# Kernel tuning notes

Hardware: AMD Instinct MI355X
Metric: run time of the kernel (lower is better)

The kernel has to match this reference:

```python
import jax, jax.numpy as jnp
import numpy as np

DIM = 768
HEAD_DIM = 768


def setup_inputs() -> dict:
    key = jax.random.key(0)
    k_x, k_w, k_b = jax.random.split(key, 3)
    x = jax.random.normal(k_x, (4, 4096, DIM), dtype=jnp.float32)
    # torch Linear(dim, 3*head_dim): weight [3H, dim]; store transposed [dim, 3H]
    scale = 1.0 / np.sqrt(DIM)
    W_qkv = jax.random.uniform(k_w, (DIM, 3 * HEAD_DIM), dtype=jnp.float32,
                               minval=-scale, maxval=scale)
    b_qkv = jax.random.uniform(k_b, (3 * HEAD_DIM,), dtype=jnp.float32,
                               minval=-scale, maxval=scale)
    return {"x": x, "W_qkv": W_qkv, "b_qkv": b_qkv}


def reference(x, W_qkv, b_qkv):
    # x: [B, N, C]
    qkv = jnp.einsum("bnc,ch->bnh", x, W_qkv) + b_qkv  # [B, N, 3H]
    q, k, v = jnp.split(qkv, 3, axis=-1)               # each [B, N, H]
    H = q.shape[-1]
    scores = jnp.einsum("bnh,bmh->bnm", q, k) / jnp.sqrt(jnp.float32(H))
    attn = jax.nn.softmax(scores, axis=-1)             # [B, N, N]
    out = jnp.einsum("bnm,bmh->bnh", attn, v)          # [B, N, H]
    return out
```

## Files before the change

kernel.cpp:

```cpp
#include <hip/hip_runtime.h>
#include <stdint.h>

typedef __attribute__((ext_vector_type(8))) short short8;
typedef __attribute__((ext_vector_type(4))) float f32x4;

#define DIM 768
#define H3 2304
#define SEQ 4096
#define NTOK 16384

__device__ __forceinline__ unsigned short f2bf(float f) {
  union { float f; uint32_t u; } c; c.f = f;
  uint32_t u = c.u;
  u += 0x7FFFu + ((u >> 16) & 1u);
  return (unsigned short)(u >> 16);
}

__device__ __forceinline__ void async_cp16(const void* g, void* l) {
  __builtin_amdgcn_global_load_lds(
      (__attribute__((address_space(1))) void*)(void*)g,
      (__attribute__((address_space(3))) void*)l, 16, 0, 0);
}

__device__ __forceinline__ void gemm_nt64(
    const unsigned short* __restrict__ A, const unsigned short* __restrict__ B,
    int K, int ldA, int ldB,
    unsigned short* As, unsigned short* Bs, f32x4 acc[4][4])
{
  const int tid = threadIdx.x, lane = tid & 63, wid = tid >> 6;
  const int wm = (wid & 1) << 6, wn = (wid >> 1) << 6;
  const int lr = lane & 15, q = lane >> 4;

#pragma unroll
  for (int i = 0; i < 4; ++i)
#pragma unroll
    for (int j = 0; j < 4; ++j)
      acc[i][j] = (f32x4){0.f, 0.f, 0.f, 0.f};

  const unsigned short* gA[4];
  const unsigned short* gB[4];
#pragma unroll
  for (int t = 0; t < 4; ++t) {
    const int c = tid + 256 * t;
    const int row = c >> 3, sc = c & 7;
    const int col8 = ((sc ^ (row & 7)) << 3);
    gA[t] = A + (size_t)row * ldA + col8;
    gB[t] = B + (size_t)row * ldB + col8;
  }

  for (int k0 = 0; k0 < K; k0 += 64) {
#pragma unroll
    for (int t = 0; t < 4; ++t)
      async_cp16(gA[t] + k0, As + (tid + 256 * t) * 8);
#pragma unroll
    for (int t = 0; t < 4; ++t)
      async_cp16(gB[t] + k0, Bs + (tid + 256 * t) * 8);
    __syncthreads();

    short8 af[4][2], bfr[4][2];
#pragma unroll
    for (int i = 0; i < 4; ++i) {
      const int ra = wm + i * 16 + lr;
#pragma unroll
      for (int s2 = 0; s2 < 2; ++s2)
        af[i][s2] = *(const short8*)(As + ra * 64 + (((s2 * 4 + q) ^ (ra & 7)) << 3));
    }
#pragma unroll
    for (int j = 0; j < 4; ++j) {
      const int rb = wn + j * 16 + lr;
#pragma unroll
      for (int s2 = 0; s2 < 2; ++s2)
        bfr[j][s2] = *(const short8*)(Bs + rb * 64 + (((s2 * 4 + q) ^ (rb & 7)) << 3));
    }
#pragma unroll
    for (int s2 = 0; s2 < 2; ++s2)
#pragma unroll
      for (int i = 0; i < 4; ++i)
#pragma unroll
        for (int j = 0; j < 4; ++j)
          acc[i][j] = __builtin_amdgcn_mfma_f32_16x16x32_bf16(af[i][s2], bfr[j][s2], acc[i][j], 0, 0, 0);
    __syncthreads();
  }
}

__global__ __launch_bounds__(256) void k_cvt(const float* __restrict__ in,
                                             unsigned short* __restrict__ o) {
  int i = blockIdx.x * 256 + threadIdx.x;
  float4 f = ((const float4*)in)[i];
  ushort4 u;
  u.x = f2bf(f.x); u.y = f2bf(f.y); u.z = f2bf(f.z); u.w = f2bf(f.w);
  ((ushort4*)o)[i] = u;
}

__global__ __launch_bounds__(256) void k_transpose(const float* __restrict__ W,
                                                   unsigned short* __restrict__ Wt) {
  __shared__ float tile[32][33];
  const int bc = blockIdx.x * 32;
  const int br = blockIdx.y * 32;
  const int tx = threadIdx.x & 31, ty = threadIdx.x >> 5;
#pragma unroll
  for (int i = 0; i < 32; i += 8)
    tile[ty + i][tx] = W[(size_t)(br + ty + i) * H3 + bc + tx];
  __syncthreads();
#pragma unroll
  for (int i = 0; i < 32; i += 8)
    Wt[(size_t)(bc + ty + i) * DIM + br + tx] = f2bf(tile[tx][ty + i]);
}

__global__ __launch_bounds__(256) void k_qkv(
    const unsigned short* __restrict__ xbf, const unsigned short* __restrict__ Wt,
    const float* __restrict__ bias,
    unsigned short* __restrict__ qb, unsigned short* __restrict__ kb,
    unsigned short* __restrict__ vT)
{
  __shared__ unsigned short As[128 * 64];
  __shared__ unsigned short Bs[128 * 64];
  f32x4 acc[4][4];
  const int g = blockIdx.x;
  const int xcd = g & 7, slot = g >> 3;
  const int tn = slot % 18, grp = slot / 18;
  const int tm = xcd + 8 * grp;
  gemm_nt64(xbf + (size_t)(tm * 128) * DIM, Wt + (size_t)(tn * 128) * DIM,
            DIM, DIM, DIM, As, Bs, acc);

  const int tid = threadIdx.x, lane = tid & 63, wid = tid >> 6;
  const int wm = (wid & 1) << 6, wn = (wid >> 1) << 6;
  const float scale = 0.036084391824351615f;
#pragma unroll
  for (int i = 0; i < 4; ++i) {
#pragma unroll
    for (int j = 0; j < 4; ++j) {
      const int col  = tn * 128 + wn + j * 16 + (lane & 15);
      const int row0 = tm * 128 + wm + i * 16 + ((lane >> 4) << 2);
      const float bc = bias[col];
#pragma unroll
      for (int r = 0; r < 4; ++r) {
        const int row = row0 + r;
        const float v = acc[i][j][r] + bc;
        if (col < 768) {
          qb[(size_t)row * DIM + col] = f2bf(v * scale);
        } else if (col < 1536) {
          kb[(size_t)row * DIM + (col - 768)] = f2bf(v);
        } else {
          const int b = row >> 12, n = row & 4095;
          vT[((size_t)b * DIM + (col - 1536)) * SEQ + n] = f2bf(v);
        }
      }
    }
  }
}

__global__ __launch_bounds__(256) void k_scores(
    const unsigned short* __restrict__ qb, const unsigned short* __restrict__ kb,
    unsigned short* __restrict__ S)
{
  __shared__ unsigned short As[128 * 64];
  __shared__ unsigned short Bs[128 * 64];
  f32x4 acc[4][4];
  const int g = blockIdx.x;
  const int xcd = g & 7, slot = g >> 3;
  const int tn = slot & 31, grp = slot >> 5;
  const int s  = xcd + 8 * grp;
  const int ty = s & 31, b = s >> 5;
  const unsigned short* A  = qb + (size_t)b * SEQ * DIM + (size_t)(ty * 128) * DIM;
  const unsigned short* Bm = kb + (size_t)b * SEQ * DIM + (size_t)(tn * 128) * DIM;
  unsigned short* Sb = S + (size_t)b * SEQ * SEQ;
  gemm_nt64(A, Bm, DIM, DIM, DIM, As, Bs, acc);

  const int tid = threadIdx.x, lane = tid & 63, wid = tid >> 6;
  const int wm = (wid & 1) << 6, wn = (wid >> 1) << 6;
#pragma unroll
  for (int i = 0; i < 4; ++i)
#pragma unroll
    for (int j = 0; j < 4; ++j) {
      const int col  = tn * 128 + wn + j * 16 + (lane & 15);
      const int row0 = ty * 128 + wm + i * 16 + ((lane >> 4) << 2);
#pragma unroll
      for (int r = 0; r < 4; ++r)
        Sb[(size_t)(row0 + r) * SEQ + col] = f2bf(acc[i][j][r]);
    }
}

__global__ __launch_bounds__(256) void k_softmax(unsigned short* __restrict__ S)
{
  const size_t base = (size_t)blockIdx.x * SEQ;
  uint4* rp = (uint4*)(S + base);
  const int t = threadIdx.x, lane = t & 63, wid = t >> 6;
  const uint4 cA = rp[t], cB = rp[t + 256];
  uint32_t wsv[8] = {cA.x, cA.y, cA.z, cA.w, cB.x, cB.y, cB.z, cB.w};
  float v[16];
#pragma unroll
  for (int i = 0; i < 8; ++i) {
    union { uint32_t u; float f; } lo, hi;
    lo.u = wsv[i] << 16; hi.u = wsv[i] & 0xFFFF0000u;
    v[2 * i] = lo.f; v[2 * i + 1] = hi.f;
  }
  float m = -1e30f;
#pragma unroll
  for (int i = 0; i < 16; ++i) m = fmaxf(m, v[i]);
#pragma unroll
  for (int off = 32; off > 0; off >>= 1) m = fmaxf(m, __shfl_down(m, off));
  __shared__ float redm[4], reds[4];
  if (lane == 0) redm[wid] = m;
  __syncthreads();
  m = fmaxf(fmaxf(redm[0], redm[1]), fmaxf(redm[2], redm[3]));
  float s = 0.f;
#pragma unroll
  for (int i = 0; i < 16; ++i) { v[i] = __expf(v[i] - m); s += v[i]; }
#pragma unroll
  for (int off = 32; off > 0; off >>= 1) s += __shfl_down(s, off);
  if (lane == 0) reds[wid] = s;
  __syncthreads();
  s = reds[0] + reds[1] + reds[2] + reds[3];
  const float inv = 1.0f / s;
  uint32_t o[8];
#pragma unroll
  for (int i = 0; i < 8; ++i)
    o[i] = (uint32_t)f2bf(v[2 * i] * inv) | ((uint32_t)f2bf(v[2 * i + 1] * inv) << 16);
  uint4 oA = {o[0], o[1], o[2], o[3]}, oB = {o[4], o[5], o[6], o[7]};
  rp[t] = oA; rp[t + 256] = oB;
}

__global__ __launch_bounds__(256) void k_pv(
    const unsigned short* __restrict__ P, const unsigned short* __restrict__ vT,
    float* __restrict__ out)
{
  __shared__ unsigned short As[128 * 64];
  __shared__ unsigned short Bs[128 * 64];
  f32x4 acc[4][4];
  const int g = blockIdx.x;
  const int xcd = g & 7, slot = g >> 3;
  const int tn = slot % 6, grp = slot / 6;
  const int s  = xcd + 8 * grp;
  const int ty = s & 31, b = s >> 5;

  const unsigned short* A  = P  + (size_t)b * SEQ * SEQ + (size_t)(ty * 128) * SEQ;
  const unsigned short* Bm = vT + (size_t)b * DIM * SEQ + (size_t)(tn * 128) * SEQ;
  float* ob = out + (size_t)b * SEQ * DIM;
  gemm_nt64(A, Bm, SEQ, SEQ, SEQ, As, Bs, acc);

  const int tid = threadIdx.x, lane = tid & 63, wid = tid >> 6;
  const int wm = (wid & 1) << 6, wn = (wid >> 1) << 6;
#pragma unroll
  for (int i = 0; i < 4; ++i)
#pragma unroll
    for (int j = 0; j < 4; ++j) {
      const int col  = tn * 128 + wn + j * 16 + (lane & 15);
      const int row0 = ty * 128 + wm + i * 16 + ((lane >> 4) << 2);
#pragma unroll
      for (int r = 0; r < 4; ++r)
        ob[(size_t)(row0 + r) * DIM + col] = acc[i][j][r];
    }
}

extern "C" void kernel_launch(void* const* d_in, const int* in_sizes, int n_in,
                              void* d_out, int out_size, void* d_ws, size_t ws_size,
                              hipStream_t stream) {
  const float* x    = (const float*)d_in[0];
  const float* W    = (const float*)d_in[1];
  const float* bias = (const float*)d_in[2];
  float* out = (float*)d_out;

  char* w = (char*)d_ws;
  unsigned short* x_bf = (unsigned short*)(w);
  unsigned short* Wt   = (unsigned short*)(w + 25165824);
  unsigned short* qb   = (unsigned short*)(w + 28704768);
  unsigned short* kb   = (unsigned short*)(w + 53870592);
  unsigned short* vT   = (unsigned short*)(w + 79036416);
  unsigned short* S    = (unsigned short*)(w + 104202240);

  k_cvt      <<<12288, 256, 0, stream>>>(x, x_bf);
  k_transpose<<<dim3(72, 24), 256, 0, stream>>>(W, Wt);
  k_qkv      <<<2304, 256, 0, stream>>>(x_bf, Wt, bias, qb, kb, vT);
  k_scores   <<<4096, 256, 0, stream>>>(qb, kb, S);
  k_softmax  <<<16384, 256, 0, stream>>>(S);
  k_pv       <<<768, 256, 0, stream>>>(S, vT, out);
}
```

Before: 512.0 us.

## Stage score tile through LDS for coalesced stores; split-K the PV GEMM

The scores kernel now writes its bf16 tile into padded shared memory and then stores it with 16-byte coalesced writes, replacing scattered 2-byte global stores. The PV GEMM is split into two halves along the key dimension, doubling the grid from 768 to 1536 blocks to fill more CUs. The second half writes to a scratch buffer that reuses the x_bf region, and an extra reduction kernel adds it into the output. This costs an extra pass over the fp32 output and one more launch.

```diff
diff --git a/kernel.cpp b/kernel.cpp
--- a/kernel.cpp
+++ b/kernel.cpp
@@ -150,12 +150,14 @@
   }
 }
 
+#define EP_LD 132
 __global__ __launch_bounds__(256) void k_scores(
     const unsigned short* __restrict__ qb, const unsigned short* __restrict__ kb,
     unsigned short* __restrict__ S)
 {
-  __shared__ unsigned short As[128 * 64];
-  __shared__ unsigned short Bs[128 * 64];
+  __shared__ unsigned short sm[128 * EP_LD];
+  unsigned short* As = sm;
+  unsigned short* Bs = sm + 128 * 64;
   f32x4 acc[4][4];
   const int g = blockIdx.x;
   const int xcd = g & 7, slot = g >> 3;
@@ -173,12 +175,20 @@
   for (int i = 0; i < 4; ++i)
 #pragma unroll
     for (int j = 0; j < 4; ++j) {
-      const int col  = tn * 128 + wn + j * 16 + (lane & 15);
-      const int row0 = ty * 128 + wm + i * 16 + ((lane >> 4) << 2);
+      const int col  = wn + j * 16 + (lane & 15);
+      const int row0 = wm + i * 16 + ((lane >> 4) << 2);
 #pragma unroll
       for (int r = 0; r < 4; ++r)
-        Sb[(size_t)(row0 + r) * SEQ + col] = f2bf(acc[i][j][r]);
-    }
+        sm[(row0 + r) * EP_LD + col] = f2bf(acc[i][j][r]);
+    }
+  __syncthreads();
+  const int rL = tid >> 4, cc = (tid & 15) << 3;
+#pragma unroll
+  for (int p = 0; p < 8; ++p) {
+    const int row = p * 16 + rL;
+    *(uint4*)(Sb + (size_t)(ty * 128 + row) * SEQ + tn * 128 + cc) =
+        *(const uint4*)(sm + row * EP_LD + cc);
+  }
 }
 
 __global__ __launch_bounds__(256) void k_softmax(unsigned short* __restrict__ S)
@@ -223,22 +233,23 @@
 
 __global__ __launch_bounds__(256) void k_pv(
     const unsigned short* __restrict__ P, const unsigned short* __restrict__ vT,
-    float* __restrict__ out)
+    float* __restrict__ out, float* __restrict__ part)
 {
   __shared__ unsigned short As[128 * 64];
   __shared__ unsigned short Bs[128 * 64];
   f32x4 acc[4][4];
   const int g = blockIdx.x;
   const int xcd = g & 7, slot = g >> 3;
-  const int tn = slot % 6, grp = slot / 6;
+  const int tn = slot % 6, t2 = slot / 6;
+  const int h = t2 & 1, grp = t2 >> 1;
   const int s  = xcd + 8 * grp;
   const int ty = s & 31, b = s >> 5;
 
-  const unsigned short* A  = P  + (size_t)b * SEQ * SEQ + (size_t)(ty * 128) * SEQ;
-  const unsigned short* Bm = vT + (size_t)b * DIM * SEQ + (size_t)(tn * 128) * SEQ;
-  float* ob = out + (size_t)b * SEQ * DIM;
-  gemm_nt64(A, Bm, SEQ, SEQ, SEQ, As, Bs, acc);
-
+  const unsigned short* A  = P  + (size_t)b * SEQ * SEQ + (size_t)(ty * 128) * SEQ + h * 2048;
+  const unsigned short* Bm = vT + (size_t)b * DIM * SEQ + (size_t)(tn * 128) * SEQ + h * 2048;
+  gemm_nt64(A, Bm, 2048, SEQ, SEQ, As, Bs, acc);
+
+  float* dst = (h ? part : out) + (size_t)b * SEQ * DIM;
   const int tid = threadIdx.x, lane = tid & 63, wid = tid >> 6;
   const int wm = (wid & 1) << 6, wn = (wid >> 1) << 6;
 #pragma unroll
@@ -249,8 +260,17 @@
       const int row0 = ty * 128 + wm + i * 16 + ((lane >> 4) << 2);
 #pragma unroll
       for (int r = 0; r < 4; ++r)
-        ob[(size_t)(row0 + r) * DIM + col] = acc[i][j][r];
-    }
+        dst[(size_t)(row0 + r) * DIM + col] = acc[i][j][r];
+    }
+}
+
+__global__ __launch_bounds__(256) void k_reduce(float* __restrict__ out,
+                                                const float* __restrict__ part) {
+  int i = blockIdx.x * 256 + threadIdx.x;
+  float4 a = ((const float4*)out)[i];
+  float4 p = ((const float4*)part)[i];
+  a.x += p.x; a.y += p.y; a.z += p.z; a.w += p.w;
+  ((float4*)out)[i] = a;
 }
 
 extern "C" void kernel_launch(void* const* d_in, const int* in_sizes, int n_in,
@@ -268,11 +288,13 @@
   unsigned short* kb   = (unsigned short*)(w + 53870592);
   unsigned short* vT   = (unsigned short*)(w + 79036416);
   unsigned short* S    = (unsigned short*)(w + 104202240);
+  float* part = (float*)(w);
 
   k_cvt      <<<12288, 256, 0, stream>>>(x, x_bf);
   k_transpose<<<dim3(72, 24), 256, 0, stream>>>(W, Wt);
   k_qkv      <<<2304, 256, 0, stream>>>(x_bf, Wt, bias, qb, kb, vT);
   k_scores   <<<4096, 256, 0, stream>>>(qb, kb, S);
   k_softmax  <<<16384, 256, 0, stream>>>(S);
-  k_pv       <<<768, 256, 0, stream>>>(S, vT, out);
-}
+  k_pv       <<<1536, 256, 0, stream>>>(S, vT, out, part);
+  k_reduce   <<<12288, 256, 0, stream>>>(out, part);
+}
```

Result: no change. 520.7 us (+1.7%).

## Fuse softmax exponentiation into score GEMM epilogue and defer normalization to PV

Applied to the files above, without the earlier changes.

Drops the separate softmax kernel. The score GEMM epilogue now applies exp to each score, accumulates per-row partial sums with atomics into a zeroed buffer, and writes the bf16 exponentials through an LDS-staged, coalesced store. The PV kernel divides its output rows by those sums. This removes a full read and write of the N×N score matrix. The cost is that exp is taken without subtracting the row max, which relies on the scores staying small enough not to overflow.

```diff
diff --git a/kernel.cpp b/kernel.cpp
--- a/kernel.cpp
+++ b/kernel.cpp
@@ -105,6 +105,10 @@
 #pragma unroll
   for (int i = 0; i < 32; i += 8)
     Wt[(size_t)(bc + ty + i) * DIM + br + tx] = f2bf(tile[tx][ty + i]);
+}
+
+__global__ __launch_bounds__(256) void k_zero(float* __restrict__ p) {
+  p[blockIdx.x * 256 + threadIdx.x] = 0.f;
 }
 
 __global__ __launch_bounds__(256) void k_qkv(
@@ -150,12 +154,14 @@
   }
 }
 
+#define EP_LD 132
 __global__ __launch_bounds__(256) void k_scores(
     const unsigned short* __restrict__ qb, const unsigned short* __restrict__ kb,
-    unsigned short* __restrict__ S)
-{
-  __shared__ unsigned short As[128 * 64];
-  __shared__ unsigned short Bs[128 * 64];
+    unsigned short* __restrict__ S, float* __restrict__ lsum)
+{
+  __shared__ unsigned short sm[128 * EP_LD];
+  unsigned short* As = sm;
+  unsigned short* Bs = sm + 128 * 64;
   f32x4 acc[4][4];
   const int g = blockIdx.x;
   const int xcd = g & 7, slot = g >> 3;
@@ -169,61 +175,47 @@
 
   const int tid = threadIdx.x, lane = tid & 63, wid = tid >> 6;
   const int wm = (wid & 1) << 6, wn = (wid >> 1) << 6;
-#pragma unroll
-  for (int i = 0; i < 4; ++i)
-#pragma unroll
-    for (int j = 0; j < 4; ++j) {
-      const int col  = tn * 128 + wn + j * 16 + (lane & 15);
-      const int row0 = ty * 128 + wm + i * 16 + ((lane >> 4) << 2);
-#pragma unroll
-      for (int r = 0; r < 4; ++r)
-        Sb[(size_t)(row0 + r) * SEQ + col] = f2bf(acc[i][j][r]);
-    }
-}
-
-__global__ __launch_bounds__(256) void k_softmax(unsigned short* __restrict__ S)
-{
-  const size_t base = (size_t)blockIdx.x * SEQ;
-  uint4* rp = (uint4*)(S + base);
-  const int t = threadIdx.x, lane = t & 63, wid = t >> 6;
-  const uint4 cA = rp[t], cB = rp[t + 256];
-  uint32_t wsv[8] = {cA.x, cA.y, cA.z, cA.w, cB.x, cB.y, cB.z, cB.w};
-  float v[16];
-#pragma unroll
-  for (int i = 0; i < 8; ++i) {
-    union { uint32_t u; float f; } lo, hi;
-    lo.u = wsv[i] << 16; hi.u = wsv[i] & 0xFFFF0000u;
-    v[2 * i] = lo.f; v[2 * i + 1] = hi.f;
-  }
-  float m = -1e30f;
-#pragma unroll
-  for (int i = 0; i < 16; ++i) m = fmaxf(m, v[i]);
-#pragma unroll
-  for (int off = 32; off > 0; off >>= 1) m = fmaxf(m, __shfl_down(m, off));
-  __shared__ float redm[4], reds[4];
-  if (lane == 0) redm[wid] = m;
+  const int q = lane >> 4;
+  float rs[4][4];
+#pragma unroll
+  for (int i = 0; i < 4; ++i) {
+#pragma unroll
+    for (int r = 0; r < 4; ++r) rs[i][r] = 0.f;
+#pragma unroll
+    for (int j = 0; j < 4; ++j) {
+      const int col  = wn + j * 16 + (lane & 15);
+      const int row0 = wm + i * 16 + (q << 2);
+#pragma unroll
+      for (int r = 0; r < 4; ++r) {
+        const float e = __expf(acc[i][j][r]);
+        sm[(row0 + r) * EP_LD + col] = f2bf(e);
+        rs[i][r] += e;
+      }
+    }
+  }
+  const int lbase = b * SEQ + ty * 128 + wm + (q << 2);
+#pragma unroll
+  for (int i = 0; i < 4; ++i)
+#pragma unroll
+    for (int r = 0; r < 4; ++r) {
+      float v = rs[i][r];
+      v += __shfl_xor(v, 1); v += __shfl_xor(v, 2);
+      v += __shfl_xor(v, 4); v += __shfl_xor(v, 8);
+      if ((lane & 15) == 0) atomicAdd(&lsum[lbase + i * 16 + r], v);
+    }
   __syncthreads();
-  m = fmaxf(fmaxf(redm[0], redm[1]), fmaxf(redm[2], redm[3]));
-  float s = 0.f;
-#pragma unroll
-  for (int i = 0; i < 16; ++i) { v[i] = __expf(v[i] - m); s += v[i]; }
-#pragma unroll
-  for (int off = 32; off > 0; off >>= 1) s += __shfl_down(s, off);
-  if (lane == 0) reds[wid] = s;
-  __syncthreads();
-  s = reds[0] + reds[1] + reds[2] + reds[3];
-  const float inv = 1.0f / s;
-  uint32_t o[8];
-#pragma unroll
-  for (int i = 0; i < 8; ++i)
-    o[i] = (uint32_t)f2bf(v[2 * i] * inv) | ((uint32_t)f2bf(v[2 * i + 1] * inv) << 16);
-  uint4 oA = {o[0], o[1], o[2], o[3]}, oB = {o[4], o[5], o[6], o[7]};
-  rp[t] = oA; rp[t + 256] = oB;
+  const int rL = tid >> 4, cc = (tid & 15) << 3;
+#pragma unroll
+  for (int p = 0; p < 8; ++p) {
+    const int row = p * 16 + rL;
+    *(uint4*)(Sb + (size_t)(ty * 128 + row) * SEQ + tn * 128 + cc) =
+        *(const uint4*)(sm + row * EP_LD + cc);
+  }
 }
 
 __global__ __launch_bounds__(256) void k_pv(
     const unsigned short* __restrict__ P, const unsigned short* __restrict__ vT,
-    float* __restrict__ out)
+    const float* __restrict__ lsum, float* __restrict__ out)
 {
   __shared__ unsigned short As[128 * 64];
   __shared__ unsigned short Bs[128 * 64];
@@ -241,15 +233,23 @@
 
   const int tid = threadIdx.x, lane = tid & 63, wid = tid >> 6;
   const int wm = (wid & 1) << 6, wn = (wid >> 1) << 6;
+  const int q = lane >> 4;
+  const int lbase = b * SEQ + ty * 128 + wm + (q << 2);
+  float inv[4][4];
+#pragma unroll
+  for (int i = 0; i < 4; ++i)
+#pragma unroll
+    for (int r = 0; r < 4; ++r)
+      inv[i][r] = 1.0f / lsum[lbase + i * 16 + r];
 #pragma unroll
   for (int i = 0; i < 4; ++i)
 #pragma unroll
     for (int j = 0; j < 4; ++j) {
       const int col  = tn * 128 + wn + j * 16 + (lane & 15);
-      const int row0 = ty * 128 + wm + i * 16 + ((lane >> 4) << 2);
+      const int row0 = ty * 128 + wm + i * 16 + (q << 2);
 #pragma unroll
       for (int r = 0; r < 4; ++r)
-        ob[(size_t)(row0 + r) * DIM + col] = acc[i][j][r];
+        ob[(size_t)(row0 + r) * DIM + col] = acc[i][j][r] * inv[i][r];
     }
 }
 
@@ -268,11 +268,12 @@
   unsigned short* kb   = (unsigned short*)(w + 53870592);
   unsigned short* vT   = (unsigned short*)(w + 79036416);
   unsigned short* S    = (unsigned short*)(w + 104202240);
+  float* lsum = (float*)(w);
 
   k_cvt      <<<12288, 256, 0, stream>>>(x, x_bf);
   k_transpose<<<dim3(72, 24), 256, 0, stream>>>(W, Wt);
   k_qkv      <<<2304, 256, 0, stream>>>(x_bf, Wt, bias, qb, kb, vT);
-  k_scores   <<<4096, 256, 0, stream>>>(qb, kb, S);
-  k_softmax  <<<16384, 256, 0, stream>>>(S);
-  k_pv       <<<768, 256, 0, stream>>>(S, vT, out);
-}
+  k_zero     <<<64, 256, 0, stream>>>(lsum);
+  k_scores   <<<4096, 256, 0, stream>>>(qb, kb, S, lsum);
+  k_pv       <<<768, 256, 0, stream>>>(S, vT, lsum, out);
+}
```

Result: slower. 543.7 us (+6.2%).
